# Kernel tuning notes

Measured on AMD Instinct MI355X. Metric: run time of the kernel, lower is better.

## Reference

```python
import jax, jax.numpy as jnp
import numpy as np

H, K_CHUNKS = 16, 16          # z_num = (h, k)
Z_DIM = 64
OC, IC, KW = 128, 128, 3      # per-chunk out, in, kernel width
HID = 256
O, I = H * OC, K_CHUNKS * IC  # 2048, 2048
L = 3
N_PDE, D_PDE = 1024, 64


def setup_inputs() -> dict:
    key = jax.random.key(0)
    ks = jax.random.split(key, 10)
    def rn(k, shape, scale=1.0):
        return jax.random.normal(k, shape, dtype=jnp.float32) * scale
    return {
        "Z": rn(ks[0], (H * K_CHUNKS, Z_DIM)),                 # stacked z_list (fmod(randn,2) ~ randn)
        "z_bias": rn(ks[1], (O,)),
        "unet_1d_weights": rn(ks[2], (O, I, L), 0.02),
        "unet_1d_bias": rn(ks[3], (O,), 0.02),
        "pde_inputs": rn(ks[4], (N_PDE, D_PDE)),
        "W1": rn(ks[5], (Z_DIM, HID), 1.0 / np.sqrt(Z_DIM)),
        "U1": rn(ks[6], (D_PDE, HID), 1.0 / np.sqrt(D_PDE)),
        "b1": jnp.zeros((HID,), jnp.float32),
        "W2": rn(ks[7], (HID, OC * IC * KW), 1.0 / np.sqrt(HID)),
        "b2": jnp.zeros((OC * IC * KW,), jnp.float32),
    }


def reference(Z, z_bias, unet_1d_weights, unet_1d_bias, pde_inputs, W1, U1, b1, W2, b2):
    # Batched hypernet: replaces the h*k sequential hyper_net calls.
    pde_feat = pde_inputs.mean(axis=0) @ U1                    # [HID], shared conditioning
    hidden = jnp.tanh(Z @ W1 + pde_feat + b1)                  # [h*k, HID]
    w = (hidden @ W2 + b2).reshape(H, K_CHUNKS, OC, IC, KW)    # per-chunk weights
    # cat over j along dim=1 (in-channels), then over i along dim=0 (out-channels)
    exe_unet_weight = w.transpose(0, 2, 1, 3, 4).reshape(O, I, KW)  # [O, I, K]
    w_2d = jnp.einsum('oik,oil->oikl', exe_unet_weight, unet_1d_weights)  # [O, I, K, L]
    bb = z_bias + unet_1d_bias                                 # [O]
    return (w_2d, bb)
```

## Files before the change

### kernel.cpp

```cpp
#include <hip/hip_runtime.h>
#include <hip/hip_bf16.h>
#include <math.h>

#define H_ 16
#define KC_ 16
#define ZD_ 64
#define HID_ 256
#define O_ 2048
#define NW2_ 49152
#define W2D_OUT 37748736
#define DPDE_ 64

typedef short bf16x8 __attribute__((ext_vector_type(8)));
typedef float f32x4 __attribute__((ext_vector_type(4)));

static __device__ __forceinline__ unsigned short f2bf(float f) {
    union { float f; unsigned u; } v; v.f = f;
    unsigned r = v.u + 0x7FFF + ((v.u >> 16) & 1);
    return (unsigned short)(r >> 16);
}

static __device__ __forceinline__ unsigned pack2(float lo, float hi) {
    return (unsigned)f2bf(lo) | ((unsigned)f2bf(hi) << 16);
}

__global__ void prep_kernel(const float* __restrict__ Z,
                            const float* __restrict__ pde,
                            const float* __restrict__ W1,
                            const float* __restrict__ U1,
                            const float* __restrict__ b1,
                            const float* __restrict__ z_bias,
                            const float* __restrict__ u_bias,
                            unsigned short* __restrict__ hiddenA,
                            float* __restrict__ out_bb) {
    __shared__ float part[16][64];
    __shared__ float meanv[64];
    __shared__ float zr[64];
    const int t = threadIdx.x, m = blockIdx.x;
    if (t < 64) zr[t] = Z[m * ZD_ + t];
    const int c4 = t & 15, rg = t >> 4;
    float sx = 0.f, sy = 0.f, sz = 0.f, sw = 0.f;
    const float4* p = (const float4*)pde;
    for (int r = 0; r < 64; ++r) {
        float4 v = p[(rg * 64 + r) * 16 + c4];
        sx += v.x; sy += v.y; sz += v.z; sw += v.w;
    }
    part[rg][c4 * 4 + 0] = sx; part[rg][c4 * 4 + 1] = sy;
    part[rg][c4 * 4 + 2] = sz; part[rg][c4 * 4 + 3] = sw;
    __syncthreads();
    if (t < 64) {
        float a = 0.f;
        #pragma unroll
        for (int g = 0; g < 16; ++g) a += part[g][t];
        meanv[t] = a * (1.f / 1024.f);
    }
    __syncthreads();
    float f = b1[t];
    #pragma unroll
    for (int d = 0; d < 64; ++d) f = fmaf(meanv[d], U1[d * HID_ + t], f);
    float s = f;
    #pragma unroll
    for (int d = 0; d < 64; ++d) s = fmaf(zr[d], W1[d * HID_ + t], s);
    hiddenA[((size_t)(t >> 3) * 256 + m) * 8 + (t & 7)] = f2bf(tanhf(s));
    if (m < 8) {
        const int idx = m * 256 + t;
        out_bb[idx] = z_bias[idx] + u_bias[idx];
    }
}

#define BT_S2 132
#define WL_ST 97
#define WL_SZ 1552

__global__ __launch_bounds__(512, 4)
void gemm_expand(const unsigned short* __restrict__ hiddenA,
                 const float* __restrict__ W2,
                 const float* __restrict__ b2,
                 const float* __restrict__ unet,
                 float* __restrict__ out) {
    __shared__ unsigned bT[96 * BT_S2];

    const int t = threadIdx.x;
    const int lane = t & 63;
    const int wave = t >> 6;
    const int n15 = lane & 15;
    const int quad = lane >> 4;
    const int L = lane & 31;
    const int half = lane >> 5;
    const int oc = blockIdx.x >> 2;
    const int icq = blockIdx.x & 3;
    const int n0g = oc * 384 + icq * 96;

    #pragma unroll
    for (int i = 0; i < 6; ++i) {
        const int u  = i * 512 + t;
        const int kp = u / 24;
        const int nq = u - kp * 24;
        const float* p0 = W2 + (size_t)(2 * kp) * NW2_ + n0g + nq * 4;
        const float4 va = *(const float4*)p0;
        const float4 vb = *(const float4*)(p0 + NW2_);
        const int kpx = kp ^ ((nq & 7) << 1) ^ (((nq >> 3) & 1) << 4);
        unsigned* r0 = &bT[(4 * nq) * BT_S2 + kpx];
        r0[0 * BT_S2] = pack2(va.x, vb.x);
        r0[1 * BT_S2] = pack2(va.y, vb.y);
        r0[2 * BT_S2] = pack2(va.z, vb.z);
        r0[3 * BT_S2] = pack2(va.w, vb.w);
    }
    __syncthreads();

    f32x4 acc[2][6];
    #pragma unroll
    for (int a = 0; a < 2; ++a)
        #pragma unroll
        for (int b = 0; b < 6; ++b) acc[a][b] = (f32x4){0.f, 0.f, 0.f, 0.f};

    #pragma unroll
    for (int ks = 0; ks < 8; ++ks) {
        const int g = ks * 4 + quad;
        bf16x8 afr[2];
        #pragma unroll
        for (int mi = 0; mi < 2; ++mi)
            afr[mi] = *(const bf16x8*)(hiddenA +
                      ((size_t)g * 256 + (wave * 2 + mi) * 16 + n15) * 8);
        const int base4 = ks * 16 + quad * 4;
        #pragma unroll
        for (int nt = 0; nt < 6; ++nt) {
            const int n = nt * 16 + n15;
            const int nqr = n >> 2;
            const int swz = ((nqr & 7) << 1) ^ (((nqr >> 3) & 1) << 4);
            const unsigned* row = &bT[n * BT_S2];
            union { bf16x8 v; unsigned long long q[2]; } bb;
            bb.q[0] = *(const unsigned long long*)&row[(base4)     ^ swz];
            bb.q[1] = *(const unsigned long long*)&row[(base4 + 2) ^ swz];
            acc[0][nt] = __builtin_amdgcn_mfma_f32_16x16x32_bf16(afr[0], bb.v, acc[0][nt], 0, 0, 0);
            acc[1][nt] = __builtin_amdgcn_mfma_f32_16x16x32_bf16(afr[1], bb.v, acc[1][nt], 0, 0, 0);
        }
    }

    float gb2v[6];
    #pragma unroll
    for (int nt = 0; nt < 6; ++nt) gb2v[nt] = b2[n0g + nt * 16 + n15];

    __syncthreads();

    float* wl = ((float*)bT) + wave * WL_SZ;

    #pragma unroll
    for (int mi = 0; mi < 2; ++mi) {
        #pragma unroll
        for (int nt = 0; nt < 6; ++nt)
            #pragma unroll
            for (int r = 0; r < 4; ++r)
                wl[(quad * 4 + r) * WL_ST + nt * 16 + n15] = acc[mi][nt][r] + gb2v[nt];

        const int o = (wave * 2 + mi) * 128 + oc;
        const float* uo = unet + (size_t)o * 6144;
        float* ob = out + (size_t)o * 18432;

        #pragma unroll
        for (int kp = 0; kp < 8; ++kp) {
            const int kc = kp * 2 + half;
            const float* wrow = wl + kc * WL_ST;
            const float* ub = uo + kc * 384 + icq * 96;
            float* os = ob + kc * 1152 + icq * 288;
            #pragma unroll
            for (int j = 0; j < 9; ++j) {
                const int d  = j * 32 + L;
                const int d3 = d / 3;
                const int d9 = d / 9;
                const int l  = d - 3 * d3;
                os[d] = wrow[d3] * ub[d9 * 3 + l];
            }
        }
    }
}

extern "C" void kernel_launch(void* const* d_in, const int* in_sizes, int n_in,
                              void* d_out, int out_size, void* d_ws, size_t ws_size,
                              hipStream_t stream) {
    const float* Z       = (const float*)d_in[0];
    const float* z_bias  = (const float*)d_in[1];
    const float* unet_w  = (const float*)d_in[2];
    const float* unet_b  = (const float*)d_in[3];
    const float* pde     = (const float*)d_in[4];
    const float* W1      = (const float*)d_in[5];
    const float* U1      = (const float*)d_in[6];
    const float* b1      = (const float*)d_in[7];
    const float* W2      = (const float*)d_in[8];
    const float* b2      = (const float*)d_in[9];
    float* out = (float*)d_out;

    unsigned short* hiddenA = (unsigned short*)d_ws;

    prep_kernel<<<256, 256, 0, stream>>>(Z, pde, W1, U1, b1, z_bias, unet_b,
                                         hiddenA, out + W2D_OUT);
    gemm_expand<<<512, 512, 0, stream>>>(hiddenA, W2, b2, unet_w, out);
}
```

Before: 277.8 us.

## Split fused GEMM-expand into separate GEMM and vectorized expand kernels

Replaces the fused GEMM-plus-expand kernel with two kernels when the workspace is large enough. The first writes the generated weight matrix in [O, I*K] layout to workspace. The second streams the outer product with unet weights using 16-byte nontemporal stores, one float4 per thread per step. This is meant to fix the scalar, poorly coalesced stores of the fused epilogue and raise occupancy for the write-bound expansion. In exchange it adds a 50MB workspace round trip (write then read of the weight buffer) and an extra kernel launch.

After: 294.6 us. 1.06x slower.

```diff
diff --git a/kernel.cpp b/kernel.cpp
--- a/kernel.cpp
+++ b/kernel.cpp
@@ -10,6 +10,8 @@
 #define NW2_ 49152
 #define W2D_OUT 37748736
 #define DPDE_ 64
+#define WSW_OFF 131072
+#define WS_NEED 50462720
 
 typedef short bf16x8 __attribute__((ext_vector_type(8)));
 typedef float f32x4 __attribute__((ext_vector_type(4)));
@@ -69,6 +71,113 @@
 }
 
 #define BT_S2 132
+
+__global__ __launch_bounds__(512, 4)
+void gemm_w(const unsigned short* __restrict__ hiddenA,
+            const float* __restrict__ W2,
+            const float* __restrict__ b2,
+            float* __restrict__ wout) {
+    __shared__ unsigned bT[96 * BT_S2];
+
+    const int t = threadIdx.x;
+    const int lane = t & 63;
+    const int wave = t >> 6;
+    const int n15 = lane & 15;
+    const int quad = lane >> 4;
+    const int oc = blockIdx.x >> 2;
+    const int icq = blockIdx.x & 3;
+    const int n0g = oc * 384 + icq * 96;
+
+    #pragma unroll
+    for (int i = 0; i < 6; ++i) {
+        const int u  = i * 512 + t;
+        const int kp = u / 24;
+        const int nq = u - kp * 24;
+        const float* p0 = W2 + (size_t)(2 * kp) * NW2_ + n0g + nq * 4;
+        const float4 va = *(const float4*)p0;
+        const float4 vb = *(const float4*)(p0 + NW2_);
+        const int kpx = kp ^ ((nq & 7) << 1) ^ (((nq >> 3) & 1) << 4);
+        unsigned* r0 = &bT[(4 * nq) * BT_S2 + kpx];
+        r0[0 * BT_S2] = pack2(va.x, vb.x);
+        r0[1 * BT_S2] = pack2(va.y, vb.y);
+        r0[2 * BT_S2] = pack2(va.z, vb.z);
+        r0[3 * BT_S2] = pack2(va.w, vb.w);
+    }
+    __syncthreads();
+
+    f32x4 acc[2][6];
+    #pragma unroll
+    for (int a = 0; a < 2; ++a)
+        #pragma unroll
+        for (int b = 0; b < 6; ++b) acc[a][b] = (f32x4){0.f, 0.f, 0.f, 0.f};
+
+    #pragma unroll
+    for (int ks = 0; ks < 8; ++ks) {
+        const int g = ks * 4 + quad;
+        bf16x8 afr[2];
+        #pragma unroll
+        for (int mi = 0; mi < 2; ++mi)
+            afr[mi] = *(const bf16x8*)(hiddenA +
+                      ((size_t)g * 256 + (wave * 2 + mi) * 16 + n15) * 8);
+        const int base4 = ks * 16 + quad * 4;
+        #pragma unroll
+        for (int nt = 0; nt < 6; ++nt) {
+            const int n = nt * 16 + n15;
+            const int nqr = n >> 2;
+            const int swz = ((nqr & 7) << 1) ^ (((nqr >> 3) & 1) << 4);
+            const unsigned* row = &bT[n * BT_S2];
+            union { bf16x8 v; unsigned long long q[2]; } bb;
+            bb.q[0] = *(const unsigned long long*)&row[(base4)     ^ swz];
+            bb.q[1] = *(const unsigned long long*)&row[(base4 + 2) ^ swz];
+            acc[0][nt] = __builtin_amdgcn_mfma_f32_16x16x32_bf16(afr[0], bb.v, acc[0][nt], 0, 0, 0);
+            acc[1][nt] = __builtin_amdgcn_mfma_f32_16x16x32_bf16(afr[1], bb.v, acc[1][nt], 0, 0, 0);
+        }
+    }
+
+    float gb2v[6];
+    #pragma unroll
+    for (int nt = 0; nt < 6; ++nt) gb2v[nt] = b2[n0g + nt * 16 + n15];
+
+    #pragma unroll
+    for (int mi = 0; mi < 2; ++mi) {
+        const int o = (wave * 2 + mi) * 128 + oc;
+        float* wb = wout + (size_t)o * 6144 + icq * 96;
+        #pragma unroll
+        for (int nt = 0; nt < 6; ++nt)
+            #pragma unroll
+            for (int r = 0; r < 4; ++r)
+                wb[(quad * 4 + r) * 384 + nt * 16 + n15] = acc[mi][nt][r] + gb2v[nt];
+    }
+}
+
+__global__ __launch_bounds__(256, 4)
+void expand(const float* __restrict__ w,
+            const float* __restrict__ unet,
+            float* __restrict__ out) {
+    const unsigned t = threadIdx.x;
+    const unsigned W0 = blockIdx.x * 9216u + t * 4u;
+    #pragma unroll
+    for (int s = 0; s < 9; ++s) {
+        const unsigned W = W0 + (unsigned)s * 1024u;
+        const unsigned q   = W / 3u;
+        const unsigned rem = W - q * 3u;
+        const unsigned i0  = W / 9u;
+        const unsigned m9  = W - i0 * 9u;
+        const float w0 = w[q];
+        const float w1 = w[q + 1u];
+        f32x4 r;
+        #pragma unroll
+        for (int c = 0; c < 4; ++c) {
+            const float wv = ((unsigned)c < 3u - rem) ? w0 : w1;
+            unsigned lc = rem + (unsigned)c;
+            if (lc >= 3u) lc -= 3u;
+            const unsigned ui = (i0 + ((m9 + (unsigned)c) >= 9u ? 1u : 0u)) * 3u + lc;
+            r[c] = wv * unet[ui];
+        }
+        __builtin_nontemporal_store(r, (f32x4*)(out + W));
+    }
+}
+
 #define WL_ST 97
 #define WL_SZ 1552
 
@@ -194,5 +303,12 @@
 
     prep_kernel<<<256, 256, 0, stream>>>(Z, pde, W1, U1, b1, z_bias, unet_b,
                                          hiddenA, out + W2D_OUT);
-    gemm_expand<<<512, 512, 0, stream>>>(hiddenA, W2, b2, unet_w, out);
-}
+
+    if (ws_size >= (size_t)WS_NEED) {
+        float* wbuf = (float*)((char*)d_ws + WSW_OFF);
+        gemm_w<<<512, 512, 0, stream>>>(hiddenA, W2, b2, wbuf);
+        expand<<<4096, 256, 0, stream>>>(wbuf, unet_w, out);
+    } else {
+        gemm_expand<<<512, 512, 0, stream>>>(hiddenA, W2, b2, unet_w, out);
+    }
+}
```

## Halve gemm tile width and vectorize output stores as float4

Applied to the files above, without the earlier changes.

The expand kernel now uses blocks of 256 threads, each covering 48 columns instead of 96. Each wave computes four M-subtiles by three N-tiles instead of two by six, and the grid doubles to 1024 blocks. The output epilogue is rewritten so that each lane writes one 16-byte float4 covering four consecutive outputs, replacing scalar strided stores, which targets the store-bandwidth-bound 150MB output. Each unet value is still loaded as a scalar, and the index arithmetic gets more complex.

Measured after the change: 365.2 us. 1.31x slower.

```diff
diff --git a/kernel.cpp b/kernel.cpp
--- a/kernel.cpp
+++ b/kernel.cpp
@@ -2,14 +2,10 @@
 #include <hip/hip_bf16.h>
 #include <math.h>
 
-#define H_ 16
-#define KC_ 16
 #define ZD_ 64
 #define HID_ 256
-#define O_ 2048
 #define NW2_ 49152
 #define W2D_OUT 37748736
-#define DPDE_ 64
 
 typedef short bf16x8 __attribute__((ext_vector_type(8)));
 typedef float f32x4 __attribute__((ext_vector_type(4)));
@@ -69,33 +65,31 @@
 }
 
 #define BT_S2 132
-#define WL_ST 97
-#define WL_SZ 1552
-
-__global__ __launch_bounds__(512, 4)
+#define WL_ST 49
+#define WL_SZ 784
+
+__global__ __launch_bounds__(256, 4)
 void gemm_expand(const unsigned short* __restrict__ hiddenA,
                  const float* __restrict__ W2,
                  const float* __restrict__ b2,
                  const float* __restrict__ unet,
                  float* __restrict__ out) {
-    __shared__ unsigned bT[96 * BT_S2];
+    __shared__ unsigned bT[48 * BT_S2];
 
     const int t = threadIdx.x;
     const int lane = t & 63;
     const int wave = t >> 6;
     const int n15 = lane & 15;
     const int quad = lane >> 4;
-    const int L = lane & 31;
-    const int half = lane >> 5;
-    const int oc = blockIdx.x >> 2;
-    const int icq = blockIdx.x & 3;
-    const int n0g = oc * 384 + icq * 96;
+    const int oc = blockIdx.x >> 3;
+    const int ics = blockIdx.x & 7;
+    const int n0g = oc * 384 + ics * 48;
 
     #pragma unroll
     for (int i = 0; i < 6; ++i) {
-        const int u  = i * 512 + t;
-        const int kp = u / 24;
-        const int nq = u - kp * 24;
+        const int u  = i * 256 + t;
+        const int kp = u / 12;
+        const int nq = u - kp * 12;
         const float* p0 = W2 + (size_t)(2 * kp) * NW2_ + n0g + nq * 4;
         const float4 va = *(const float4*)p0;
         const float4 vb = *(const float4*)(p0 + NW2_);
@@ -108,23 +102,23 @@
     }
     __syncthreads();
 
-    f32x4 acc[2][6];
-    #pragma unroll
-    for (int a = 0; a < 2; ++a)
-        #pragma unroll
-        for (int b = 0; b < 6; ++b) acc[a][b] = (f32x4){0.f, 0.f, 0.f, 0.f};
+    f32x4 acc[4][3];
+    #pragma unroll
+    for (int a = 0; a < 4; ++a)
+        #pragma unroll
+        for (int b = 0; b < 3; ++b) acc[a][b] = (f32x4){0.f, 0.f, 0.f, 0.f};
 
     #pragma unroll
     for (int ks = 0; ks < 8; ++ks) {
         const int g = ks * 4 + quad;
-        bf16x8 afr[2];
-        #pragma unroll
-        for (int mi = 0; mi < 2; ++mi)
+        bf16x8 afr[4];
+        #pragma unroll
+        for (int mi = 0; mi < 4; ++mi)
             afr[mi] = *(const bf16x8*)(hiddenA +
-                      ((size_t)g * 256 + (wave * 2 + mi) * 16 + n15) * 8);
+                      ((size_t)g * 256 + (wave * 4 + mi) * 16 + n15) * 8);
         const int base4 = ks * 16 + quad * 4;
         #pragma unroll
-        for (int nt = 0; nt < 6; ++nt) {
+        for (int nt = 0; nt < 3; ++nt) {
             const int n = nt * 16 + n15;
             const int nqr = n >> 2;
             const int swz = ((nqr & 7) << 1) ^ (((nqr >> 3) & 1) << 4);
@@ -132,45 +126,56 @@
             union { bf16x8 v; unsigned long long q[2]; } bb;
             bb.q[0] = *(const unsigned long long*)&row[(base4)     ^ swz];
             bb.q[1] = *(const unsigned long long*)&row[(base4 + 2) ^ swz];
-            acc[0][nt] = __builtin_amdgcn_mfma_f32_16x16x32_bf16(afr[0], bb.v, acc[0][nt], 0, 0, 0);
-            acc[1][nt] = __builtin_amdgcn_mfma_f32_16x16x32_bf16(afr[1], bb.v, acc[1][nt], 0, 0, 0);
+            #pragma unroll
+            for (int mi = 0; mi < 4; ++mi)
+                acc[mi][nt] = __builtin_amdgcn_mfma_f32_16x16x32_bf16(afr[mi], bb.v, acc[mi][nt], 0, 0, 0);
         }
     }
 
-    float gb2v[6];
-    #pragma unroll
-    for (int nt = 0; nt < 6; ++nt) gb2v[nt] = b2[n0g + nt * 16 + n15];
+    float gb2v[3];
+    #pragma unroll
+    for (int nt = 0; nt < 3; ++nt) gb2v[nt] = b2[n0g + nt * 16 + n15];
 
     __syncthreads();
 
     float* wl = ((float*)bT) + wave * WL_SZ;
 
     #pragma unroll
-    for (int mi = 0; mi < 2; ++mi) {
-        #pragma unroll
-        for (int nt = 0; nt < 6; ++nt)
+    for (int mi = 0; mi < 4; ++mi) {
+        #pragma unroll
+        for (int nt = 0; nt < 3; ++nt)
             #pragma unroll
             for (int r = 0; r < 4; ++r)
                 wl[(quad * 4 + r) * WL_ST + nt * 16 + n15] = acc[mi][nt][r] + gb2v[nt];
 
-        const int o = (wave * 2 + mi) * 128 + oc;
-        const float* uo = unet + (size_t)o * 6144;
-        float* ob = out + (size_t)o * 18432;
-
-        #pragma unroll
-        for (int kp = 0; kp < 8; ++kp) {
-            const int kc = kp * 2 + half;
+        const int o = (wave * 4 + mi) * 128 + oc;
+        const float* uo = unet + (size_t)o * 6144 + ics * 48;
+        float* ob = out + (size_t)o * 18432 + ics * 144;
+
+        #pragma unroll
+        for (int it = 0; it < 9; ++it) {
+            const int u  = it * 64 + lane;
+            const int kc = u / 36;
+            const int rq = u - kc * 36;
+            const int r  = rq * 4;
             const float* wrow = wl + kc * WL_ST;
-            const float* ub = uo + kc * 384 + icq * 96;
-            float* os = ob + kc * 1152 + icq * 288;
+            const float* ub   = uo + kc * 384;
+            const int c0 = r / 3;
+            const int rm = r - c0 * 3;
+            const int i0 = r / 9;
+            const int m9 = r - i0 * 9;
+            const float w0 = wrow[c0];
+            const float w1 = wrow[c0 + 1];
+            f32x4 v;
             #pragma unroll
-            for (int j = 0; j < 9; ++j) {
-                const int d  = j * 32 + L;
-                const int d3 = d / 3;
-                const int d9 = d / 9;
-                const int l  = d - 3 * d3;
-                os[d] = wrow[d3] * ub[d9 * 3 + l];
+            for (int c = 0; c < 4; ++c) {
+                const float wv = (rm + c < 3) ? w0 : w1;
+                int lc = rm + c;
+                if (lc >= 3) lc -= 3;
+                const int ui = (i0 + ((m9 + c) >= 9 ? 1 : 0)) * 3 + lc;
+                v[c] = wv * ub[ui];
             }
+            *(f32x4*)(ob + kc * 1152 + r) = v;
         }
     }
 }
@@ -194,5 +199,5 @@
 
     prep_kernel<<<256, 256, 0, stream>>>(Z, pde, W1, U1, b1, z_bias, unet_b,
                                          hiddenA, out + W2D_OUT);
-    gemm_expand<<<512, 512, 0, stream>>>(hiddenA, W2, b2, unet_w, out);
-}
+    gemm_expand<<<1024, 256, 0, stream>>>(hiddenA, W2, b2, unet_w, out);
+}
```
